# Performance work log

Hardware: AMD Instinct MI355X
Metric: run time of the kernel (lower is better)

Reference implementation:

```python
import jax, jax.numpy as jnp
import numpy as np

BS, T, NOBJ = 16, 32, 100
GLOVE, GEMB, ADIM, GCN_DIM, H, ASPACE, RES = 300, 64, 10, 512, 512, 6, 512


def setup_inputs() -> dict:
    key = jax.random.key(0)
    ks = jax.random.split(key, 34)
    rn = lambda k, shp, s=0.02: (jax.random.normal(k, shp, jnp.float32) * s)
    inp = {}
    inp["target"] = jax.random.normal(ks[0], (BS, T, GLOVE), jnp.float32)
    inp["input_"] = jax.random.normal(ks[1], (BS, T, RES, 1, 1), jnp.float32)
    inp["action_probs"] = jax.random.uniform(ks[2], (BS, T, ASPACE), jnp.float32)
    # symmetric normalized adjacency (D^-1/2 A D^-1/2), as normalize_adj produces
    A_raw = (jax.random.uniform(ks[3], (NOBJ, NOBJ)) < 0.1).astype(jnp.float32)
    A_raw = ((A_raw + A_raw.T + jnp.eye(NOBJ)) > 0).astype(jnp.float32)
    dinv = 1.0 / jnp.sqrt(jnp.sum(A_raw, axis=1))
    inp["A"] = A_raw * dinv[:, None] * dinv[None, :]
    inp["all_glove"] = jax.random.normal(ks[4], (NOBJ, GLOVE), jnp.float32)
    inp["Wword"] = rn(ks[5], (GEMB, GLOVE)); inp["bword"] = jnp.zeros((GEMB,))
    inp["Wg"] = rn(ks[6], (GEMB, GLOVE)); inp["bg"] = jnp.zeros((GEMB,))
    inp["Wa"] = rn(ks[7], (ADIM, ASPACE)); inp["ba"] = jnp.zeros((ADIM,))
    inp["W0"] = rn(ks[8], (256, RES + GEMB))
    inp["W1"] = rn(ks[9], (256, 256))
    inp["W2"] = rn(ks[10], (1, 256))
    inp["Wfm"] = rn(ks[11], (GCN_DIM, NOBJ)); inp["bfm"] = jnp.zeros((GCN_DIM,))
    fused_in = RES + GEMB + ADIM + GCN_DIM
    inp["Wf"] = rn(ks[12], (H, fused_in)); inp["bf"] = jnp.zeros((H,))
    inp["Wih"] = rn(ks[13], (4 * H, H)); inp["Whh"] = rn(ks[14], (4 * H, H))
    inp["bih"] = jnp.zeros((4 * H,)); inp["bhh"] = jnp.zeros((4 * H,))
    inp["Wa1"] = rn(ks[15], (128, H)); inp["ba1"] = jnp.zeros((128,))
    inp["Wa2"] = rn(ks[16], (ASPACE, 128)); inp["ba2"] = jnp.zeros((ASPACE,))
    inp["Wc1"] = rn(ks[17], (128, H)); inp["bc1"] = jnp.zeros((128,))
    inp["Wc2"] = rn(ks[18], (1, 128)); inp["bc2"] = jnp.zeros((1,))
    return inp


def _forward(target, input_, action_probs, A, all_glove, Wword, bword, Wg, bg,
             Wa, ba, W0, W1, W2, Wfm, bfm, Wf, bf, Wih, Whh, bih, bhh,
             Wa1, ba1, Wa2, ba2, Wc1, bc1, Wc2, bc2):
    bs, t = target.shape[0], target.shape[1]
    B = bs * t
    feats = input_.reshape(B, RES)                      # [B,512] (squeeze 1x1)
    glove_e = jax.nn.relu(target.reshape(B, GLOVE) @ Wg.T + bg)
    act_e = jax.nn.relu(action_probs.reshape(B, ASPACE) @ Wa.T + ba)
    # GCN branch (all_glove is detached in the original)
    word = jax.lax.stop_gradient(all_glove) @ Wword.T + bword   # [N,GEMB]
    N = A.shape[0]
    class_e = jnp.broadcast_to(feats[:, None, :], (B, N, RES))
    x = jnp.concatenate([class_e, jnp.broadcast_to(word[None], (B, N, GEMB))], -1)
    x = jax.nn.relu(jnp.einsum('nm,bmd->bnd', A, x) @ W0.T)     # [B,N,256]
    x = jax.nn.relu(jnp.einsum('nm,bmd->bnd', A, x) @ W1.T)     # [B,N,256]
    x = jax.nn.relu(jnp.einsum('nm,bmd->bnd', A, x) @ W2.T)     # [B,N,1]
    gcn_e = x[..., 0] @ Wfm.T + bfm                             # [B,GCN_DIM]
    fused = jnp.concatenate([feats, glove_e, act_e, gcn_e], -1)
    out = jax.nn.relu(fused @ Wf.T + bf).reshape(bs, t, H)
    # LSTM (torch gate order i,f,g,o), batch_first, zero init state
    h0 = jnp.zeros((bs, H), out.dtype)
    c0 = jnp.zeros((bs, H), out.dtype)
    def step(carry, xt):
        h, c = carry
        g = xt @ Wih.T + h @ Whh.T + bih + bhh
        i, f, gg, o = jnp.split(g, 4, axis=-1)
        c = jax.nn.sigmoid(f) * c + jax.nn.sigmoid(i) * jnp.tanh(gg)
        h = jax.nn.sigmoid(o) * jnp.tanh(c)
        return (h, c), h
    (hT, cT), hs = jax.lax.scan(step, (h0, c0), out.transpose(1, 0, 2))
    sf = hs.transpose(1, 0, 2).reshape(B, H)
    actor = jax.nn.relu(jax.nn.relu(sf @ Wa1.T + ba1) @ Wa2.T + ba2).reshape(bs, t, ASPACE)
    critic = jax.nn.relu(jax.nn.relu(sf @ Wc1.T + bc1) @ Wc2.T + bc2).reshape(bs, t, 1)
    return actor, critic, hT[None], cT[None]


def reference(target, input_, action_probs, A, all_glove, Wword, bword, Wg, bg,
              Wa, ba, W0, W1, W2, Wfm, bfm, Wf, bf, Wih, Whh, bih, bhh,
              Wa1, ba1, Wa2, ba2, Wc1, bc1, Wc2, bc2):
    return _forward(target, input_, action_probs, A, all_glove, Wword, bword,
                    Wg, bg, Wa, ba, W0, W1, W2, Wfm, bfm, Wf, bf, Wih, Whh,
                    bih, bhh, Wa1, ba1, Wa2, ba2, Wc1, bc1, Wc2, bc2)
```

## Files before the change

kernel.cpp:

```cpp
#include <hip/hip_runtime.h>
#include <cmath>

constexpr int BSZ = 16, T = 32, NOBJ = 100;
constexpr int GLOVE = 300, GEMB = 64, ADIM = 10, GCN_DIM = 512, Hh = 512, ASPACE = 6, RES = 512;
constexpr int Bt = BSZ * T;
constexpr int FUSED_IN = RES + GEMB + ADIM + GCN_DIM;
constexpr int FP = 1120;

typedef __attribute__((ext_vector_type(8))) short bf16x8;
typedef __attribute__((ext_vector_type(4))) float f32x4;

__device__ __forceinline__ unsigned short f2bf(float f) {
    unsigned u = __float_as_uint(f);
    return (unsigned short)((u + 0x7FFFu + ((u >> 16) & 1u)) >> 16);
}
__device__ __forceinline__ unsigned pk2(float a, float b) {
    return (unsigned)f2bf(a) | ((unsigned)f2bf(b) << 16);
}
__device__ __forceinline__ float sigf(float x) { return 1.f / (1.f + __expf(-x)); }

template<bool RELU, int OMODE>
__global__ __launch_bounds__(256)
void mgemm(const unsigned short* __restrict__ A, int lda,
           const unsigned short* __restrict__ B, int ldb,
           float* __restrict__ Cf, unsigned short* __restrict__ Cb, int ldc,
           const float* __restrict__ bias, int K)
{
    const int tid = threadIdx.x;
    const int l = tid & 63, wv = tid >> 6;
    const int m0 = blockIdx.y * 64 + wv * 16;
    const int n0 = blockIdx.x * 64;
    const int lr = l & 15, kg = l >> 4;
    const unsigned short* ap = A + (long)(m0 + lr) * lda + kg * 8;
    const unsigned short* bp = B + (long)(n0 + lr) * ldb + kg * 8;
    f32x4 acc0 = (f32x4){0.f, 0.f, 0.f, 0.f};
    f32x4 acc1 = acc0, acc2 = acc0, acc3 = acc0;
    for (int k0 = 0; k0 < K; k0 += 32) {
        bf16x8 a  = *(const bf16x8*)(ap + k0);
        bf16x8 b0 = *(const bf16x8*)(bp + k0);
        bf16x8 b1 = *(const bf16x8*)(bp + 16 * ldb + k0);
        bf16x8 b2 = *(const bf16x8*)(bp + 32 * ldb + k0);
        bf16x8 b3 = *(const bf16x8*)(bp + 48 * ldb + k0);
        acc0 = __builtin_amdgcn_mfma_f32_16x16x32_bf16(a, b0, acc0, 0, 0, 0);
        acc1 = __builtin_amdgcn_mfma_f32_16x16x32_bf16(a, b1, acc1, 0, 0, 0);
        acc2 = __builtin_amdgcn_mfma_f32_16x16x32_bf16(a, b2, acc2, 0, 0, 0);
        acc3 = __builtin_amdgcn_mfma_f32_16x16x32_bf16(a, b3, acc3, 0, 0, 0);
    }
    f32x4 av[4] = {acc0, acc1, acc2, acc3};
#pragma unroll
    for (int nf = 0; nf < 4; ++nf) {
        int n = n0 + nf * 16 + lr;
        float bs = bias ? bias[n] : 0.f;
#pragma unroll
        for (int r = 0; r < 4; ++r) {
            float val = av[nf][r] + bs;
            if (RELU) val = fmaxf(val, 0.f);
            long idx = (long)(m0 + kg * 4 + r) * ldc + n;
            if (OMODE == 0) Cf[idx] = val;
            else            Cb[idx] = f2bf(val);
        }
    }
}

template<bool RELU>
__global__ __launch_bounds__(128)
void gemm32(const float* __restrict__ A, int lda,
            const float* __restrict__ B, int ldb,
            float* __restrict__ C, int ldc,
            const float* __restrict__ bias, int M, int N, int K)
{
    __shared__ float As[32][36];
    __shared__ float Bs[32][68];
    const int tid = threadIdx.x;
    const int m0 = blockIdx.y * 32, n0 = blockIdx.x * 64;
    const int mi = tid >> 4, ni = tid & 15;
    float acc[4][4] = {};
    for (int k0 = 0; k0 < K; k0 += 32) {
        __syncthreads();
#pragma unroll
        for (int l = 0; l < 2; ++l) {
            int e = tid + l * 128;
            int row = e >> 3, kq = (e & 7) << 2;
            float4 va = make_float4(0.f, 0.f, 0.f, 0.f);
            if (m0 + row < M && k0 + kq < K)
                va = *(const float4*)&A[(long)(m0 + row) * lda + k0 + kq];
            As[kq + 0][row] = va.x; As[kq + 1][row] = va.y;
            As[kq + 2][row] = va.z; As[kq + 3][row] = va.w;
        }
#pragma unroll
        for (int l = 0; l < 4; ++l) {
            int e = tid + l * 128;
            int row = e >> 3, kq = (e & 7) << 2;
            float4 vb = make_float4(0.f, 0.f, 0.f, 0.f);
            if (n0 + row < N && k0 + kq < K)
                vb = *(const float4*)&B[(long)(n0 + row) * ldb + k0 + kq];
            Bs[kq + 0][row] = vb.x; Bs[kq + 1][row] = vb.y;
            Bs[kq + 2][row] = vb.z; Bs[kq + 3][row] = vb.w;
        }
        __syncthreads();
#pragma unroll
        for (int k = 0; k < 32; ++k) {
            float4 a4 = *(const float4*)&As[k][4 * mi];
            float4 b4 = *(const float4*)&Bs[k][4 * ni];
            acc[0][0] = fmaf(a4.x, b4.x, acc[0][0]); acc[0][1] = fmaf(a4.x, b4.y, acc[0][1]);
            acc[0][2] = fmaf(a4.x, b4.z, acc[0][2]); acc[0][3] = fmaf(a4.x, b4.w, acc[0][3]);
            acc[1][0] = fmaf(a4.y, b4.x, acc[1][0]); acc[1][1] = fmaf(a4.y, b4.y, acc[1][1]);
            acc[1][2] = fmaf(a4.y, b4.z, acc[1][2]); acc[1][3] = fmaf(a4.y, b4.w, acc[1][3]);
            acc[2][0] = fmaf(a4.z, b4.x, acc[2][0]); acc[2][1] = fmaf(a4.z, b4.y, acc[2][1]);
            acc[2][2] = fmaf(a4.z, b4.z, acc[2][2]); acc[2][3] = fmaf(a4.z, b4.w, acc[2][3]);
            acc[3][0] = fmaf(a4.w, b4.x, acc[3][0]); acc[3][1] = fmaf(a4.w, b4.y, acc[3][1]);
            acc[3][2] = fmaf(a4.w, b4.z, acc[3][2]); acc[3][3] = fmaf(a4.w, b4.w, acc[3][3]);
        }
    }
    const int n = n0 + 4 * ni;
    if (n >= N) return;
    float4 bv = make_float4(0.f, 0.f, 0.f, 0.f);
    if (bias) bv = *(const float4*)&bias[n];
#pragma unroll
    for (int r = 0; r < 4; ++r) {
        int m = m0 + 4 * mi + r;
        if (m >= M) continue;
        float4 v;
        v.x = acc[r][0] + bv.x; v.y = acc[r][1] + bv.y;
        v.z = acc[r][2] + bv.z; v.w = acc[r][3] + bv.w;
        if (RELU) {
            v.x = fmaxf(v.x, 0.f); v.y = fmaxf(v.y, 0.f);
            v.z = fmaxf(v.z, 0.f); v.w = fmaxf(v.w, 0.f);
        }
        *(float4*)&C[(long)m * ldc + n] = v;
    }
}

constexpr int ZLD = 152;

__global__ __launch_bounds__(256, 2)
void gcn_fused(const float* __restrict__ u,
               const float* __restrict__ v,
               const float* __restrict__ rowsum,
               const float* __restrict__ Aglob,
               const bf16x8* __restrict__ W1f,
               const bf16x8* __restrict__ Af,
               const float* __restrict__ w2,
               unsigned short* __restrict__ x3b)
{
    __shared__ unsigned short X1s[2][112 * 40];
    __shared__ unsigned short Z1Ts[128 * ZLD];
    __shared__ float u_lds[256];
    __shared__ float rs_lds[112];
    __shared__ float w2l[256];
    __shared__ float spart[4][112];
    __shared__ float sl[112];

    const int b = blockIdx.x, tid = threadIdx.x;
    const int l = tid & 63, wv = tid >> 6;
    const int lrow = l & 15, kg = l >> 4;

    u_lds[tid] = u[(long)b * 256 + tid];
    w2l[tid] = w2[tid];
    if (tid < 112) rs_lds[tid] = (tid < 100) ? rowsum[tid] : 0.f;
    if (tid < 128) {
        uint4 z = make_uint4(0, 0, 0, 0);
        *(uint4*)&Z1Ts[tid * ZLD + 112] = z;
        *(uint4*)&Z1Ts[tid * ZLD + 120] = z;
    }
    if (tid < 28) x3b[(long)b * 128 + 100 + tid] = 0;
    __syncthreads();

    const int sn = tid >> 1;
    const int kh = (tid & 1) << 4;
    const int kq = kh >> 2;
    const bool gen = (tid < 224) && (sn < 100);
    const float4* vrow = gen ? ((const float4*)v + sn * 64) : nullptr;
    const float rsn = (tid < 224) ? rs_lds[sn] : 0.f;

    float sacc[7][4];
#pragma unroll
    for (int mt = 0; mt < 7; ++mt)
#pragma unroll
        for (int r = 0; r < 4; ++r) sacc[mt][r] = 0.f;

    for (int half = 0; half < 2; ++half) {
        f32x4 acc1[7][2];
#pragma unroll
        for (int mt = 0; mt < 7; ++mt)
#pragma unroll
            for (int jtl = 0; jtl < 2; ++jtl) acc1[mt][jtl] = (f32x4){0.f, 0.f, 0.f, 0.f};

        float4 q0, q1, q2, q3;
        if (gen) { q0 = vrow[kq]; q1 = vrow[kq + 1]; q2 = vrow[kq + 2]; q3 = vrow[kq + 3]; }

        int buf = 0;
        for (int kt = 0; kt < 8; ++kt) {
            if (tid < 224) {
                int kb = kt * 32 + kh;
                uint4 p0 = make_uint4(0, 0, 0, 0), p1 = make_uint4(0, 0, 0, 0);
                if (gen) {
                    float4 u0 = *(const float4*)&u_lds[kb];
                    float4 u1 = *(const float4*)&u_lds[kb + 4];
                    float4 u2 = *(const float4*)&u_lds[kb + 8];
                    float4 u3 = *(const float4*)&u_lds[kb + 12];
                    float x0 = fmaxf(fmaf(rsn, u0.x, q0.x), 0.f), x1 = fmaxf(fmaf(rsn, u0.y, q0.y), 0.f);
                    float x2 = fmaxf(fmaf(rsn, u0.z, q0.z), 0.f), x3v = fmaxf(fmaf(rsn, u0.w, q0.w), 0.f);
                    float x4 = fmaxf(fmaf(rsn, u1.x, q1.x), 0.f), x5 = fmaxf(fmaf(rsn, u1.y, q1.y), 0.f);
                    float x6 = fmaxf(fmaf(rsn, u1.z, q1.z), 0.f), x7 = fmaxf(fmaf(rsn, u1.w, q1.w), 0.f);
                    float x8 = fmaxf(fmaf(rsn, u2.x, q2.x), 0.f), x9 = fmaxf(fmaf(rsn, u2.y, q2.y), 0.f);
                    float xa = fmaxf(fmaf(rsn, u2.z, q2.z), 0.f), xb = fmaxf(fmaf(rsn, u2.w, q2.w), 0.f);
                    float xc = fmaxf(fmaf(rsn, u3.x, q3.x), 0.f), xd = fmaxf(fmaf(rsn, u3.y, q3.y), 0.f);
                    float xe = fmaxf(fmaf(rsn, u3.z, q3.z), 0.f), xf = fmaxf(fmaf(rsn, u3.w, q3.w), 0.f);
                    p0 = make_uint4(pk2(x0, x1), pk2(x2, x3v), pk2(x4, x5), pk2(x6, x7));
                    p1 = make_uint4(pk2(x8, x9), pk2(xa, xb), pk2(xc, xd), pk2(xe, xf));
                }
                *(uint4*)&X1s[buf][sn * 40 + kh] = p0;
                *(uint4*)&X1s[buf][sn * 40 + kh + 8] = p1;
            }
            float4 n0q, n1q, n2q, n3q;
            if (kt < 7 && gen) {
                int base = (kt + 1) * 8 + kq;
                n0q = vrow[base]; n1q = vrow[base + 1]; n2q = vrow[base + 2]; n3q = vrow[base + 3];
            }
            __syncthreads();
            bf16x8 af[7];
#pragma unroll
            for (int mt = 0; mt < 7; ++mt)
                af[mt] = *(const bf16x8*)&X1s[buf][(mt * 16 + lrow) * 40 + kg * 8];
#pragma unroll
            for (int jtl = 0; jtl < 2; ++jtl) {
                int jt = half * 8 + wv * 2 + jtl;
                bf16x8 bfr = W1f[(jt * 8 + kt) * 64 + l];
#pragma unroll
                for (int mt = 0; mt < 7; ++mt)
                    acc1[mt][jtl] = __builtin_amdgcn_mfma_f32_16x16x32_bf16(af[mt], bfr, acc1[mt][jtl], 0, 0, 0);
            }
            q0 = n0q; q1 = n1q; q2 = n2q; q3 = n3q;
            buf ^= 1;
        }

#pragma unroll
        for (int mt = 0; mt < 7; ++mt)
#pragma unroll
            for (int jtl = 0; jtl < 2; ++jtl) {
                int jloc = (wv * 2 + jtl) * 16 + lrow;
                f32x4 a = acc1[mt][jtl];
                uint2 zz;
                zz.x = pk2(a[0], a[1]);
                zz.y = pk2(a[2], a[3]);
                *(uint2*)&Z1Ts[jloc * ZLD + mt * 16 + kg * 4] = zz;
            }

        bf16x8 bz[2][4];
#pragma unroll
        for (int jtl = 0; jtl < 2; ++jtl)
#pragma unroll
            for (int k2 = 0; k2 < 4; ++k2)
                bz[jtl][k2] = *(const bf16x8*)&Z1Ts[((wv * 2 + jtl) * 16 + lrow) * ZLD + k2 * 32 + kg * 8];
#pragma unroll
        for (int mt = 0; mt < 7; ++mt) {
            bf16x8 aA[4];
#pragma unroll
            for (int k2 = 0; k2 < 4; ++k2) aA[k2] = Af[(mt * 4 + k2) * 64 + l];
#pragma unroll
            for (int jtl = 0; jtl < 2; ++jtl) {
                f32x4 p = (f32x4){0.f, 0.f, 0.f, 0.f};
#pragma unroll
                for (int k2 = 0; k2 < 4; ++k2)
                    p = __builtin_amdgcn_mfma_f32_16x16x32_bf16(aA[k2], bz[jtl][k2], p, 0, 0, 0);
                float w2j = w2l[half * 128 + (wv * 2 + jtl) * 16 + lrow];
#pragma unroll
                for (int r = 0; r < 4; ++r)
                    sacc[mt][r] = fmaf(fmaxf(p[r], 0.f), w2j, sacc[mt][r]);
            }
        }
    }

#pragma unroll
    for (int mt = 0; mt < 7; ++mt) {
        float s0 = sacc[mt][0], s1 = sacc[mt][1], s2 = sacc[mt][2], s3 = sacc[mt][3];
#pragma unroll
        for (int off = 1; off < 16; off <<= 1) {
            s0 += __shfl_xor(s0, off);
            s1 += __shfl_xor(s1, off);
            s2 += __shfl_xor(s2, off);
            s3 += __shfl_xor(s3, off);
        }
        if (lrow == 0) {
            int m = mt * 16 + kg * 4;
            spart[wv][m + 0] = s0; spart[wv][m + 1] = s1;
            spart[wv][m + 2] = s2; spart[wv][m + 3] = s3;
        }
    }
    __syncthreads();
    if (tid < 112)
        sl[tid] = spart[0][tid] + spart[1][tid] + spart[2][tid] + spart[3][tid];
    __syncthreads();

    float sv0 = (l < 100) ? sl[l] : 0.f;
    float sv1 = (l + 64 < 100) ? sl[l + 64] : 0.f;
#pragma unroll 5
    for (int i = 0; i < 25; ++i) {
        int n = i * 4 + wv;
        float a0 = (l < 100) ? Aglob[n * 100 + l] : 0.f;
        float a1 = (l + 64 < 100) ? Aglob[n * 100 + l + 64] : 0.f;
        float p = a0 * sv0 + a1 * sv1;
#pragma unroll
        for (int off = 32; off; off >>= 1) p += __shfl_xor(p, off);
        if (l == 0) x3b[(long)b * 128 + n] = f2bf(fmaxf(p, 0.f));
    }
}

__global__ __launch_bounds__(256)
void lstm_mf(const float* __restrict__ xWih,
             const bf16x8* __restrict__ Whhf,
             const unsigned short* __restrict__ hPrev,
             unsigned short* __restrict__ hNext,
             float* __restrict__ cBuf,
             float* __restrict__ hFin,
             unsigned short* __restrict__ sfb, int t)
{
    __shared__ float gl[4][16][17];
    const int tid = threadIdx.x;
    const int l = tid & 63, g = tid >> 6;
    const int bid = blockIdx.x;
    const int jt = g * 32 + bid;
    const int lr = l & 15, kg = l >> 4;
    const unsigned short* hp = hPrev + lr * 512 + kg * 8;
    const bf16x8* wp = Whhf + (size_t)jt * 16 * 64 + l;
    f32x4 acc = (f32x4){0.f, 0.f, 0.f, 0.f};
#pragma unroll
    for (int kt = 0; kt < 16; ++kt) {
        bf16x8 a = *(const bf16x8*)(hp + kt * 32);
        acc = __builtin_amdgcn_mfma_f32_16x16x32_bf16(a, wp[kt * 64], acc, 0, 0, 0);
    }
#pragma unroll
    for (int r = 0; r < 4; ++r) gl[g][kg * 4 + r][lr] = acc[r];
    __syncthreads();
    const int b = tid >> 4, jl = tid & 15;
    const int jh = bid * 16 + jl;
    const float* xw = xWih + (size_t)(b * T + t) * 2048;
    float gi = gl[0][b][jl] + xw[jh];
    float gf = gl[1][b][jl] + xw[512 + jh];
    float gg = gl[2][b][jl] + xw[1024 + jh];
    float go = gl[3][b][jl] + xw[1536 + jh];
    float cp = cBuf[b * 512 + jh];
    float cn = sigf(gf) * cp + sigf(gi) * tanhf(gg);
    float hn = sigf(go) * tanhf(cn);
    cBuf[b * 512 + jh] = cn;
    hNext[b * 512 + jh] = f2bf(hn);
    hFin[b * 512 + jh] = hn;
    sfb[(size_t)(b * T + t) * 512 + jh] = f2bf(hn);
}

__global__ void k_aw_rowsum(const float* __restrict__ A, const float* __restrict__ word,
                            float* __restrict__ Aw, float* __restrict__ rowsum)
{
    int i = blockIdx.x * 256 + threadIdx.x;
    if (i < 6400) {
        int n = i / 64, k = i % 64;
        float s = 0.f;
        for (int m = 0; m < 100; ++m) s += A[n * 100 + m] * word[m * 64 + k];
        Aw[i] = s;
    } else if (i < 6500) {
        int n = i - 6400;
        float s = 0.f;
        for (int m = 0; m < 100; ++m) s += A[n * 100 + m];
        rowsum[n] = s;
    }
}

__global__ void k_prep(const float* __restrict__ Whh, uint4* __restrict__ Whhf,
                       const float* __restrict__ Wf, unsigned short* __restrict__ WfPb,
                       const float* __restrict__ Wih, unsigned short* __restrict__ Wihb,
                       const float* __restrict__ Wa1, const float* __restrict__ Wc1,
                       unsigned short* __restrict__ Whdb,
                       const float* __restrict__ ba1, const float* __restrict__ bc1,
                       float* __restrict__ bhd,
                       const float* __restrict__ Wg, unsigned short* __restrict__ Wgb,
                       const float* __restrict__ W0, unsigned short* __restrict__ W0ab,
                       const float* __restrict__ Wfm, unsigned short* __restrict__ Wfmb,
                       const float* __restrict__ target, unsigned short* __restrict__ tgtb,
                       const float* __restrict__ feats, unsigned short* __restrict__ featsb,
                       unsigned short* __restrict__ fusedb,
                       const float* __restrict__ aprob, const float* __restrict__ Wa,
                       const float* __restrict__ ba,
                       unsigned short* __restrict__ hbA, float* __restrict__ cBuf,
                       const float* __restrict__ bih, const float* __restrict__ bhh,
                       float* __restrict__ bsum,
                       const float* __restrict__ W1, uint4* __restrict__ W1f,
                       const float* __restrict__ A, uint4* __restrict__ Af)
{
    int bx = blockIdx.x, tid = threadIdx.x;
    if (bx < 512) {
        int job = bx * 256 + tid;
        int jtkt = job >> 6, ll = job & 63;
        int j = (jtkt >> 4) * 16 + (ll & 15);
        int k0 = (jtkt & 15) * 32 + (ll >> 4) * 8;
        const float* src = &Whh[(long)j * 512 + k0];
        uint4 p;
        p.x = pk2(src[0], src[1]); p.y = pk2(src[2], src[3]);
        p.z = pk2(src[4], src[5]); p.w = pk2(src[6], src[7]);
        Whhf[job] = p;
    } else if (bx < 2752) {
        int i = (bx - 512) * 256 + tid;
        int r = i / FP, c = i - r * FP;
        WfPb[i] = f2bf(c < FUSED_IN ? Wf[(long)r * FUSED_IN + c] : 0.f);
    } else if (bx < 6848) {
        int i = (bx - 2752) * 256 + tid;
        Wihb[i] = f2bf(Wih[i]);
    } else if (bx < 7360) {
        int i = (bx - 6848) * 256 + tid;
        int r = i >> 9, c = i & 511;
        Whdb[i] = f2bf(r < 128 ? Wa1[r * 512 + c] : Wc1[(r - 128) * 512 + c]);
    } else if (bx < 7361) {
        bhd[tid] = (tid < 128) ? ba1[tid] : bc1[tid - 128];
    } else if (bx < 7441) {
        int i = (bx - 7361) * 256 + tid;
        int r = i / 320, c = i - r * 320;
        Wgb[i] = f2bf(c < GLOVE ? Wg[r * GLOVE + c] : 0.f);
    } else if (bx < 7953) {
        int i = (bx - 7441) * 256 + tid;
        int r = i >> 9, c = i & 511;
        W0ab[i] = f2bf(W0[(long)r * 576 + c]);
    } else if (bx < 8209) {
        int i = (bx - 7953) * 256 + tid;
        int r = i >> 7, c = i & 127;
        Wfmb[i] = f2bf(c < 100 ? Wfm[r * 100 + c] : 0.f);
    } else if (bx < 8849) {
        int i = (bx - 8209) * 256 + tid;
        int r = i / 320, c = i - r * 320;
        tgtb[i] = f2bf(c < GLOVE ? target[(long)r * GLOVE + c] : 0.f);
    } else if (bx < 9873) {
        int i = (bx - 8849) * 256 + tid;
        featsb[i] = f2bf(feats[i]);
    } else if (bx < 10897) {
        int i = (bx - 9873) * 256 + tid;
        int r = i >> 9, c = i & 511;
        fusedb[(long)r * FP + c] = f2bf(feats[i]);
    } else if (bx < 10917) {
        int i = (bx - 10897) * 256 + tid;
        int r = i / 10, c6 = i - r * 10;
        float s = ba[c6];
#pragma unroll
        for (int k = 0; k < 6; ++k) s += aprob[r * 6 + k] * Wa[c6 * 6 + k];
        fusedb[(long)r * FP + 576 + c6] = f2bf(fmaxf(s, 0.f));
    } else if (bx < 10961) {
        int i = (bx - 10917) * 256 + tid;
        int r = i / 22, c = 1098 + (i - r * 22);
        fusedb[(long)r * FP + c] = 0;
    } else if (bx < 11009) {
        int sub = bx - 10961;
        if (sub < 16) { int i = sub * 256 + tid; hbA[i] = 0; }
        else          { int i = (sub - 16) * 256 + tid; cBuf[i] = 0.f; }
    } else if (bx < 11017) {
        int i = (bx - 11009) * 256 + tid;
        bsum[i] = bih[i] + bhh[i];
    } else if (bx < 11049) {
        int job = (bx - 11017) * 256 + tid;
        int jt = job >> 9, rem = job & 511, kt = rem >> 6, lane = rem & 63;
        int j = jt * 16 + (lane & 15), k0 = kt * 32 + (lane >> 4) * 8;
        const float* src = &W1[(long)j * 256 + k0];
        uint4 p;
        p.x = pk2(src[0], src[1]); p.y = pk2(src[2], src[3]);
        p.z = pk2(src[4], src[5]); p.w = pk2(src[6], src[7]);
        W1f[job] = p;
    } else {
        int job = (bx - 11049) * 256 + tid;
        int mt = job >> 8, rem = job & 255, kt = rem >> 6, lane = rem & 63;
        int m = mt * 16 + (lane & 15), n0 = kt * 32 + (lane >> 4) * 8;
        float h[8];
#pragma unroll
        for (int e = 0; e < 8; ++e)
            h[e] = (m < 100 && n0 + e < 100) ? A[m * 100 + n0 + e] : 0.f;
        uint4 p;
        p.x = pk2(h[0], h[1]); p.y = pk2(h[2], h[3]);
        p.z = pk2(h[4], h[5]); p.w = pk2(h[6], h[7]);
        Af[job] = p;
    }
}

__global__ void k_finish(const float* __restrict__ hd,
                         const float* __restrict__ Wa2, const float* __restrict__ ba2,
                         const float* __restrict__ Wc2, const float* __restrict__ bc2,
                         const float* __restrict__ hFin, const float* __restrict__ cBuf,
                         float* __restrict__ out)
{
    if (blockIdx.x < 32) {
        int row = blockIdx.x * 16 + (threadIdx.x >> 4);
        int slot = threadIdx.x & 15;
        if (slot < 6) {
            const float4* h4 = (const float4*)(hd + (long)row * 256);
            const float4* w4 = (const float4*)(Wa2 + slot * 128);
            float s = 0.f;
#pragma unroll
            for (int k = 0; k < 32; ++k) {
                float4 h = h4[k], w = w4[k];
                s += h.x * w.x + h.y * w.y + h.z * w.z + h.w * w.w;
            }
            out[row * 6 + slot] = fmaxf(s + ba2[slot], 0.f);
        } else if (slot == 6) {
            const float4* h4 = (const float4*)(hd + (long)row * 256 + 128);
            const float4* w4 = (const float4*)(Wc2);
            float s = 0.f;
#pragma unroll
            for (int k = 0; k < 32; ++k) {
                float4 h = h4[k], w = w4[k];
                s += h.x * w.x + h.y * w.y + h.z * w.z + h.w * w.w;
            }
            out[3072 + row] = fmaxf(s + bc2[0], 0.f);
        }
    } else {
        int i = (blockIdx.x - 32) * 256 + threadIdx.x;
        out[3584 + i] = hFin[i];
        out[11776 + i] = cBuf[i];
    }
}

static inline void mg(hipStream_t st, const unsigned short* A, int lda,
                      const unsigned short* B, int ldb,
                      float* Cf, unsigned short* Cb, int ldc,
                      const float* bias, int M, int N, int K, bool relu, bool bf16out)
{
    dim3 g(N / 64, M / 64), blk(256);
    if (bf16out) {
        if (relu) hipLaunchKernelGGL((mgemm<true, 1>), g, blk, 0, st, A, lda, B, ldb, Cf, Cb, ldc, bias, K);
        else      hipLaunchKernelGGL((mgemm<false, 1>), g, blk, 0, st, A, lda, B, ldb, Cf, Cb, ldc, bias, K);
    } else {
        if (relu) hipLaunchKernelGGL((mgemm<true, 0>), g, blk, 0, st, A, lda, B, ldb, Cf, Cb, ldc, bias, K);
        else      hipLaunchKernelGGL((mgemm<false, 0>), g, blk, 0, st, A, lda, B, ldb, Cf, Cb, ldc, bias, K);
    }
}
static inline void g32(hipStream_t st, const float* A, int lda, const float* B, int ldb,
                       float* C, int ldc, const float* bias, int M, int N, int K, bool relu)
{
    dim3 g((N + 63) / 64, (M + 31) / 32), blk(128);
    if (relu) hipLaunchKernelGGL((gemm32<true>), g, blk, 0, st, A, lda, B, ldb, C, ldc, bias, M, N, K);
    else      hipLaunchKernelGGL((gemm32<false>), g, blk, 0, st, A, lda, B, ldb, C, ldc, bias, M, N, K);
}

extern "C" void kernel_launch(void* const* d_in, const int* in_sizes, int n_in,
                              void* d_out, int out_size, void* d_ws, size_t ws_size,
                              hipStream_t stream)
{
    const float* target = (const float*)d_in[0];
    const float* input_ = (const float*)d_in[1];
    const float* aprob  = (const float*)d_in[2];
    const float* Adj    = (const float*)d_in[3];
    const float* aglove = (const float*)d_in[4];
    const float* Wword  = (const float*)d_in[5];
    const float* bword  = (const float*)d_in[6];
    const float* Wg     = (const float*)d_in[7];
    const float* bg     = (const float*)d_in[8];
    const float* Wa     = (const float*)d_in[9];
    const float* ba     = (const float*)d_in[10];
    const float* W0     = (const float*)d_in[11];
    const float* W1     = (const float*)d_in[12];
    const float* W2     = (const float*)d_in[13];
    const float* Wfm    = (const float*)d_in[14];
    const float* bfm    = (const float*)d_in[15];
    const float* Wf     = (const float*)d_in[16];
    const float* bf     = (const float*)d_in[17];
    const float* Wih    = (const float*)d_in[18];
    const float* Whh    = (const float*)d_in[19];
    const float* bih    = (const float*)d_in[20];
    const float* bhh    = (const float*)d_in[21];
    const float* Wa1    = (const float*)d_in[22];
    const float* ba1    = (const float*)d_in[23];
    const float* Wa2    = (const float*)d_in[24];
    const float* ba2    = (const float*)d_in[25];
    const float* Wc1    = (const float*)d_in[26];
    const float* bc1    = (const float*)d_in[27];
    const float* Wc2    = (const float*)d_in[28];
    const float* bc2    = (const float*)d_in[29];

    float* ws = (float*)d_ws;
    float* out = (float*)d_out;

    size_t off = 0;
    auto alloc = [&](size_t n) { size_t r = off; off += (n + 255) & ~(size_t)255; return r; };
    float* u       = ws + alloc(512 * 256);
    float* word    = ws + alloc(100 * 64);
    float* Aw      = ws + alloc(100 * 64);
    float* rowsum  = ws + alloc(128);
    float* v       = ws + alloc(100 * 256);
    float* bsum    = ws + alloc(2048);
    float* bhd     = ws + alloc(256);
    float* xWih    = ws + alloc((size_t)512 * 2048);
    float* hd      = ws + alloc(512 * 256);
    float* hFin    = ws + alloc(BSZ * Hh);
    float* cBuf    = ws + alloc(BSZ * Hh);
    float* W1frag  = ws + alloc(32768);
    float* Afrag   = ws + alloc(7168);
    float* Whhf    = ws + alloc((size_t)524288);
    unsigned short* x3b     = (unsigned short*)(ws + alloc(512 * 128 / 2));
    unsigned short* fusedb  = (unsigned short*)(ws + alloc((size_t)512 * FP / 2));
    unsigned short* WfPb    = (unsigned short*)(ws + alloc((size_t)512 * FP / 2));
    unsigned short* outfb   = (unsigned short*)(ws + alloc(512 * 512 / 2));
    unsigned short* Wihb    = (unsigned short*)(ws + alloc((size_t)2048 * 512 / 2));
    unsigned short* Whdb    = (unsigned short*)(ws + alloc(256 * 512 / 2));
    unsigned short* Wgb     = (unsigned short*)(ws + alloc(64 * 320 / 2));
    unsigned short* W0ab    = (unsigned short*)(ws + alloc(256 * 512 / 2));
    unsigned short* Wfmb    = (unsigned short*)(ws + alloc(512 * 128 / 2));
    unsigned short* tgtb    = (unsigned short*)(ws + alloc(512 * 320 / 2));
    unsigned short* featsb  = (unsigned short*)(ws + alloc(512 * 512 / 2));
    unsigned short* sfb     = (unsigned short*)(ws + alloc(512 * 512 / 2));
    unsigned short* hbA     = (unsigned short*)(ws + alloc(BSZ * Hh / 2));
    unsigned short* hbB     = (unsigned short*)(ws + alloc(BSZ * Hh / 2));
    (void)ws_size; (void)in_sizes; (void)n_in; (void)out_size;

    const float* feats = input_;

    hipLaunchKernelGGL(k_prep, dim3(11056), dim3(256), 0, stream,
                       Whh, (uint4*)Whhf, Wf, WfPb, Wih, Wihb, Wa1, Wc1, Whdb, ba1, bc1, bhd,
                       Wg, Wgb, W0, W0ab, Wfm, Wfmb, target, tgtb, feats, featsb,
                       fusedb, aprob, Wa, ba, hbA, cBuf, bih, bhh, bsum,
                       W1, (uint4*)W1frag, Adj, (uint4*)Afrag);

    g32(stream, aglove, GLOVE, Wword, GLOVE, word, 64, bword, 100, 64, GLOVE, false);
    hipLaunchKernelGGL(k_aw_rowsum, dim3(26), dim3(256), 0, stream, Adj, word, Aw, rowsum);
    g32(stream, Aw, 64, W0 + 512, 576, v, 256, nullptr, 100, 256, 64, false);

    mg(stream, featsb, 512, W0ab, 512, u, nullptr, 256, nullptr, 512, 256, 512, false, false);
    mg(stream, tgtb, 320, Wgb, 320, nullptr, fusedb + 512, FP, bg, 512, 64, 320, true, true);

    hipLaunchKernelGGL(gcn_fused, dim3(Bt), dim3(256), 0, stream,
                       u, v, rowsum, Adj, (const bf16x8*)W1frag, (const bf16x8*)Afrag, W2, x3b);
    mg(stream, x3b, 128, Wfmb, 128, nullptr, fusedb + 586, FP, bfm, 512, 512, 128, false, true);

    mg(stream, fusedb, FP, WfPb, FP, nullptr, outfb, 512, bf, 512, 512, FP, true, true);
    mg(stream, outfb, 512, Wihb, 512, xWih, nullptr, 2048, bsum, 512, 2048, 512, false, false);

    for (int t = 0; t < T; ++t) {
        const unsigned short* hp = (t & 1) ? hbB : hbA;
        unsigned short* hn = (t & 1) ? hbA : hbB;
        hipLaunchKernelGGL(lstm_mf, dim3(32), dim3(256), 0, stream,
                           xWih, (const bf16x8*)Whhf, hp, hn, cBuf, hFin, sfb, t);
    }

    mg(stream, sfb, 512, Whdb, 512, hd, nullptr, 256, bhd, 512, 256, 512, true, false);
    hipLaunchKernelGGL(k_finish, dim3(64), dim3(256), 0, stream,
                       hd, Wa2, ba2, Wc2, bc2, hFin, cBuf, out);
}
```

Measured before the change: 316.9 us.

## Persist LSTM across timesteps with grid barrier, split GCN pack, prefetch GEMM loads

The 32 per-timestep LSTM launches become a single persistent kernel. It keeps the Whh fragments and the cell state in registers and synchronises the 32 blocks through an atomic-counter grid barrier, which removes per-step launch overhead and the reloading of weights. The GCN kernel is split into a separate X1 packing kernel that writes bf16 MFMA fragments to global memory, and the core kernel reads them directly with no LDS staging or intra-loop syncs. The generic MFMA GEMM gains a 4-deep register prefetch of its operands. Risks: the spin barrier relies on all 32 blocks being co-resident, and the X1 buffer adds several MB of global traffic.

```diff
diff --git a/kernel.cpp b/kernel.cpp
--- a/kernel.cpp
+++ b/kernel.cpp
@@ -33,18 +33,39 @@
     const int lr = l & 15, kg = l >> 4;
     const unsigned short* ap = A + (long)(m0 + lr) * lda + kg * 8;
     const unsigned short* bp = B + (long)(n0 + lr) * ldb + kg * 8;
+    const int nk = K >> 5;
     f32x4 acc0 = (f32x4){0.f, 0.f, 0.f, 0.f};
     f32x4 acc1 = acc0, acc2 = acc0, acc3 = acc0;
-    for (int k0 = 0; k0 < K; k0 += 32) {
-        bf16x8 a  = *(const bf16x8*)(ap + k0);
-        bf16x8 b0 = *(const bf16x8*)(bp + k0);
-        bf16x8 b1 = *(const bf16x8*)(bp + 16 * ldb + k0);
-        bf16x8 b2 = *(const bf16x8*)(bp + 32 * ldb + k0);
-        bf16x8 b3 = *(const bf16x8*)(bp + 48 * ldb + k0);
-        acc0 = __builtin_amdgcn_mfma_f32_16x16x32_bf16(a, b0, acc0, 0, 0, 0);
-        acc1 = __builtin_amdgcn_mfma_f32_16x16x32_bf16(a, b1, acc1, 0, 0, 0);
-        acc2 = __builtin_amdgcn_mfma_f32_16x16x32_bf16(a, b2, acc2, 0, 0, 0);
-        acc3 = __builtin_amdgcn_mfma_f32_16x16x32_bf16(a, b3, acc3, 0, 0, 0);
+    bf16x8 a_[4], b0_[4], b1_[4], b2_[4], b3_[4];
+#pragma unroll
+    for (int s = 0; s < 4; ++s) {
+        if (s < nk) {
+            int k = s * 32;
+            a_[s]  = *(const bf16x8*)(ap + k);
+            b0_[s] = *(const bf16x8*)(bp + k);
+            b1_[s] = *(const bf16x8*)(bp + 16 * ldb + k);
+            b2_[s] = *(const bf16x8*)(bp + 32 * ldb + k);
+            b3_[s] = *(const bf16x8*)(bp + 48 * ldb + k);
+        }
+    }
+    for (int i = 0; i < nk; i += 4) {
+#pragma unroll
+        for (int s = 0; s < 4; ++s) {
+            if (i + s < nk) {
+                acc0 = __builtin_amdgcn_mfma_f32_16x16x32_bf16(a_[s], b0_[s], acc0, 0, 0, 0);
+                acc1 = __builtin_amdgcn_mfma_f32_16x16x32_bf16(a_[s], b1_[s], acc1, 0, 0, 0);
+                acc2 = __builtin_amdgcn_mfma_f32_16x16x32_bf16(a_[s], b2_[s], acc2, 0, 0, 0);
+                acc3 = __builtin_amdgcn_mfma_f32_16x16x32_bf16(a_[s], b3_[s], acc3, 0, 0, 0);
+                if (i + s + 4 < nk) {
+                    int k = (i + s + 4) * 32;
+                    a_[s]  = *(const bf16x8*)(ap + k);
+                    b0_[s] = *(const bf16x8*)(bp + k);
+                    b1_[s] = *(const bf16x8*)(bp + 16 * ldb + k);
+                    b2_[s] = *(const bf16x8*)(bp + 32 * ldb + k);
+                    b3_[s] = *(const bf16x8*)(bp + 48 * ldb + k);
+                }
+            }
+        }
     }
     f32x4 av[4] = {acc0, acc1, acc2, acc3};
 #pragma unroll
@@ -131,22 +152,53 @@
     }
 }
 
-constexpr int ZLD = 152;
-
-__global__ __launch_bounds__(256, 2)
-void gcn_fused(const float* __restrict__ u,
-               const float* __restrict__ v,
-               const float* __restrict__ rowsum,
-               const float* __restrict__ Aglob,
-               const bf16x8* __restrict__ W1f,
-               const bf16x8* __restrict__ Af,
-               const float* __restrict__ w2,
-               unsigned short* __restrict__ x3b)
-{
-    __shared__ unsigned short X1s[2][112 * 40];
-    __shared__ unsigned short Z1Ts[128 * ZLD];
+__global__ __launch_bounds__(256)
+void x1pack(const float* __restrict__ u, const float* __restrict__ v,
+            const float* __restrict__ rowsum, uint4* __restrict__ X1g)
+{
     __shared__ float u_lds[256];
     __shared__ float rs_lds[112];
+    const int b = blockIdx.x, tid = threadIdx.x;
+    u_lds[tid] = u[(long)b * 256 + tid];
+    if (tid < 112) rs_lds[tid] = (tid < 100) ? rowsum[tid] : 0.f;
+    __syncthreads();
+    uint4* outp = X1g + (size_t)b * 3584;
+#pragma unroll
+    for (int it = 0; it < 14; ++it) {
+        int job = it * 256 + tid;
+        int l = job & 63;
+        int kt = (job >> 6) & 7;
+        int mt = job >> 9;
+        int n = mt * 16 + (l & 15);
+        int k0 = kt * 32 + ((l >> 4) << 3);
+        uint4 p = make_uint4(0, 0, 0, 0);
+        if (n < 100) {
+            float rsn = rs_lds[n];
+            float4 u0 = *(const float4*)&u_lds[k0];
+            float4 u1 = *(const float4*)&u_lds[k0 + 4];
+            const float4* vp = (const float4*)&v[n * 256 + k0];
+            float4 v0 = vp[0], v1 = vp[1];
+            float x0 = fmaxf(fmaf(rsn, u0.x, v0.x), 0.f), x1 = fmaxf(fmaf(rsn, u0.y, v0.y), 0.f);
+            float x2 = fmaxf(fmaf(rsn, u0.z, v0.z), 0.f), x3 = fmaxf(fmaf(rsn, u0.w, v0.w), 0.f);
+            float x4 = fmaxf(fmaf(rsn, u1.x, v1.x), 0.f), x5 = fmaxf(fmaf(rsn, u1.y, v1.y), 0.f);
+            float x6 = fmaxf(fmaf(rsn, u1.z, v1.z), 0.f), x7 = fmaxf(fmaf(rsn, u1.w, v1.w), 0.f);
+            p = make_uint4(pk2(x0, x1), pk2(x2, x3), pk2(x4, x5), pk2(x6, x7));
+        }
+        outp[job] = p;
+    }
+}
+
+constexpr int ZLD = 152;
+
+__global__ __launch_bounds__(256, 2)
+void gcn_core(const bf16x8* __restrict__ X1g,
+              const float* __restrict__ Aglob,
+              const bf16x8* __restrict__ W1f,
+              const bf16x8* __restrict__ Af,
+              const float* __restrict__ w2,
+              unsigned short* __restrict__ x3b)
+{
+    __shared__ unsigned short Z1Ts[128 * ZLD];
     __shared__ float w2l[256];
     __shared__ float spart[4][112];
     __shared__ float sl[112];
@@ -155,9 +207,7 @@
     const int l = tid & 63, wv = tid >> 6;
     const int lrow = l & 15, kg = l >> 4;
 
-    u_lds[tid] = u[(long)b * 256 + tid];
     w2l[tid] = w2[tid];
-    if (tid < 112) rs_lds[tid] = (tid < 100) ? rowsum[tid] : 0.f;
     if (tid < 128) {
         uint4 z = make_uint4(0, 0, 0, 0);
         *(uint4*)&Z1Ts[tid * ZLD + 112] = z;
@@ -166,12 +216,7 @@
     if (tid < 28) x3b[(long)b * 128 + 100 + tid] = 0;
     __syncthreads();
 
-    const int sn = tid >> 1;
-    const int kh = (tid & 1) << 4;
-    const int kq = kh >> 2;
-    const bool gen = (tid < 224) && (sn < 100);
-    const float4* vrow = gen ? ((const float4*)v + sn * 64) : nullptr;
-    const float rsn = (tid < 224) ? rs_lds[sn] : 0.f;
+    const bf16x8* xb = X1g + (size_t)b * 3584 + l;
 
     float sacc[7][4];
 #pragma unroll
@@ -186,43 +231,12 @@
 #pragma unroll
             for (int jtl = 0; jtl < 2; ++jtl) acc1[mt][jtl] = (f32x4){0.f, 0.f, 0.f, 0.f};
 
-        float4 q0, q1, q2, q3;
-        if (gen) { q0 = vrow[kq]; q1 = vrow[kq + 1]; q2 = vrow[kq + 2]; q3 = vrow[kq + 3]; }
-
-        int buf = 0;
+#pragma unroll
         for (int kt = 0; kt < 8; ++kt) {
-            if (tid < 224) {
-                int kb = kt * 32 + kh;
-                uint4 p0 = make_uint4(0, 0, 0, 0), p1 = make_uint4(0, 0, 0, 0);
-                if (gen) {
-                    float4 u0 = *(const float4*)&u_lds[kb];
-                    float4 u1 = *(const float4*)&u_lds[kb + 4];
-                    float4 u2 = *(const float4*)&u_lds[kb + 8];
-                    float4 u3 = *(const float4*)&u_lds[kb + 12];
-                    float x0 = fmaxf(fmaf(rsn, u0.x, q0.x), 0.f), x1 = fmaxf(fmaf(rsn, u0.y, q0.y), 0.f);
-                    float x2 = fmaxf(fmaf(rsn, u0.z, q0.z), 0.f), x3v = fmaxf(fmaf(rsn, u0.w, q0.w), 0.f);
-                    float x4 = fmaxf(fmaf(rsn, u1.x, q1.x), 0.f), x5 = fmaxf(fmaf(rsn, u1.y, q1.y), 0.f);
-                    float x6 = fmaxf(fmaf(rsn, u1.z, q1.z), 0.f), x7 = fmaxf(fmaf(rsn, u1.w, q1.w), 0.f);
-                    float x8 = fmaxf(fmaf(rsn, u2.x, q2.x), 0.f), x9 = fmaxf(fmaf(rsn, u2.y, q2.y), 0.f);
-                    float xa = fmaxf(fmaf(rsn, u2.z, q2.z), 0.f), xb = fmaxf(fmaf(rsn, u2.w, q2.w), 0.f);
-                    float xc = fmaxf(fmaf(rsn, u3.x, q3.x), 0.f), xd = fmaxf(fmaf(rsn, u3.y, q3.y), 0.f);
-                    float xe = fmaxf(fmaf(rsn, u3.z, q3.z), 0.f), xf = fmaxf(fmaf(rsn, u3.w, q3.w), 0.f);
-                    p0 = make_uint4(pk2(x0, x1), pk2(x2, x3v), pk2(x4, x5), pk2(x6, x7));
-                    p1 = make_uint4(pk2(x8, x9), pk2(xa, xb), pk2(xc, xd), pk2(xe, xf));
-                }
-                *(uint4*)&X1s[buf][sn * 40 + kh] = p0;
-                *(uint4*)&X1s[buf][sn * 40 + kh + 8] = p1;
-            }
-            float4 n0q, n1q, n2q, n3q;
-            if (kt < 7 && gen) {
-                int base = (kt + 1) * 8 + kq;
-                n0q = vrow[base]; n1q = vrow[base + 1]; n2q = vrow[base + 2]; n3q = vrow[base + 3];
-            }
-            __syncthreads();
             bf16x8 af[7];
 #pragma unroll
             for (int mt = 0; mt < 7; ++mt)
-                af[mt] = *(const bf16x8*)&X1s[buf][(mt * 16 + lrow) * 40 + kg * 8];
+                af[mt] = xb[mt * 512 + kt * 64];
 #pragma unroll
             for (int jtl = 0; jtl < 2; ++jtl) {
                 int jt = half * 8 + wv * 2 + jtl;
@@ -231,8 +245,6 @@
                 for (int mt = 0; mt < 7; ++mt)
                     acc1[mt][jtl] = __builtin_amdgcn_mfma_f32_16x16x32_bf16(af[mt], bfr, acc1[mt][jtl], 0, 0, 0);
             }
-            q0 = n0q; q1 = n1q; q2 = n2q; q3 = n3q;
-            buf ^= 1;
         }
 
 #pragma unroll
@@ -308,13 +320,14 @@
 }
 
 __global__ __launch_bounds__(256)
-void lstm_mf(const float* __restrict__ xWih,
-             const bf16x8* __restrict__ Whhf,
-             const unsigned short* __restrict__ hPrev,
-             unsigned short* __restrict__ hNext,
-             float* __restrict__ cBuf,
-             float* __restrict__ hFin,
-             unsigned short* __restrict__ sfb, int t)
+void lstm_persist(const float* __restrict__ xWih,
+                  const bf16x8* __restrict__ Whhf,
+                  unsigned short* __restrict__ hbA,
+                  unsigned short* __restrict__ hbB,
+                  float* __restrict__ cBuf,
+                  float* __restrict__ hFin,
+                  unsigned short* __restrict__ sfb,
+                  unsigned* __restrict__ bar)
 {
     __shared__ float gl[4][16][17];
     const int tid = threadIdx.x;
@@ -322,31 +335,48 @@
     const int bid = blockIdx.x;
     const int jt = g * 32 + bid;
     const int lr = l & 15, kg = l >> 4;
-    const unsigned short* hp = hPrev + lr * 512 + kg * 8;
     const bf16x8* wp = Whhf + (size_t)jt * 16 * 64 + l;
-    f32x4 acc = (f32x4){0.f, 0.f, 0.f, 0.f};
-#pragma unroll
-    for (int kt = 0; kt < 16; ++kt) {
-        bf16x8 a = *(const bf16x8*)(hp + kt * 32);
-        acc = __builtin_amdgcn_mfma_f32_16x16x32_bf16(a, wp[kt * 64], acc, 0, 0, 0);
-    }
-#pragma unroll
-    for (int r = 0; r < 4; ++r) gl[g][kg * 4 + r][lr] = acc[r];
-    __syncthreads();
-    const int b = tid >> 4, jl = tid & 15;
+    bf16x8 w[16];
+#pragma unroll
+    for (int kt = 0; kt < 16; ++kt) w[kt] = wp[kt * 64];
+    const int fb = tid >> 4, jl = tid & 15;
     const int jh = bid * 16 + jl;
-    const float* xw = xWih + (size_t)(b * T + t) * 2048;
-    float gi = gl[0][b][jl] + xw[jh];
-    float gf = gl[1][b][jl] + xw[512 + jh];
-    float gg = gl[2][b][jl] + xw[1024 + jh];
-    float go = gl[3][b][jl] + xw[1536 + jh];
-    float cp = cBuf[b * 512 + jh];
-    float cn = sigf(gf) * cp + sigf(gi) * tanhf(gg);
-    float hn = sigf(go) * tanhf(cn);
-    cBuf[b * 512 + jh] = cn;
-    hNext[b * 512 + jh] = f2bf(hn);
-    hFin[b * 512 + jh] = hn;
-    sfb[(size_t)(b * T + t) * 512 + jh] = f2bf(hn);
+    float c_reg = 0.f;
+    const unsigned short* hprev = hbA;
+    unsigned short* hnext = hbB;
+    for (int t = 0; t < T; ++t) {
+        const unsigned short* hp = hprev + lr * 512 + kg * 8;
+        f32x4 acc = (f32x4){0.f, 0.f, 0.f, 0.f};
+#pragma unroll
+        for (int kt = 0; kt < 16; ++kt) {
+            bf16x8 a = *(const bf16x8*)(hp + kt * 32);
+            acc = __builtin_amdgcn_mfma_f32_16x16x32_bf16(a, w[kt], acc, 0, 0, 0);
+        }
+#pragma unroll
+        for (int r = 0; r < 4; ++r) gl[g][kg * 4 + r][lr] = acc[r];
+        __syncthreads();
+        const float* xw = xWih + (size_t)(fb * T + t) * 2048;
+        float gi = gl[0][fb][jl] + xw[jh];
+        float gf = gl[1][fb][jl] + xw[512 + jh];
+        float gg = gl[2][fb][jl] + xw[1024 + jh];
+        float go = gl[3][fb][jl] + xw[1536 + jh];
+        float cn = sigf(gf) * c_reg + sigf(gi) * tanhf(gg);
+        float hn = sigf(go) * tanhf(cn);
+        c_reg = cn;
+        hnext[fb * 512 + jh] = f2bf(hn);
+        sfb[(size_t)(fb * T + t) * 512 + jh] = f2bf(hn);
+        if (t == T - 1) { hFin[fb * 512 + jh] = hn; cBuf[fb * 512 + jh] = cn; }
+        __syncthreads();
+        if (tid == 0) {
+            __threadfence();
+            atomicAdd(bar, 1u);
+            unsigned target = 32u * (unsigned)(t + 1);
+            while (atomicAdd(bar, 0u) < target) { }
+            __threadfence();
+        }
+        __syncthreads();
+        const unsigned short* tmp = hprev; hprev = hnext; hnext = (unsigned short*)tmp;
+    }
 }
 
 __global__ void k_aw_rowsum(const float* __restrict__ A, const float* __restrict__ word,
@@ -381,7 +411,7 @@
                        unsigned short* __restrict__ fusedb,
                        const float* __restrict__ aprob, const float* __restrict__ Wa,
                        const float* __restrict__ ba,
-                       unsigned short* __restrict__ hbA, float* __restrict__ cBuf,
+                       unsigned short* __restrict__ hbA, unsigned* __restrict__ bar,
                        const float* __restrict__ bih, const float* __restrict__ bhh,
                        float* __restrict__ bsum,
                        const float* __restrict__ W1, uint4* __restrict__ W1f,
@@ -445,15 +475,16 @@
         int i = (bx - 10917) * 256 + tid;
         int r = i / 22, c = 1098 + (i - r * 22);
         fusedb[(long)r * FP + c] = 0;
-    } else if (bx < 11009) {
-        int sub = bx - 10961;
-        if (sub < 16) { int i = sub * 256 + tid; hbA[i] = 0; }
-        else          { int i = (sub - 16) * 256 + tid; cBuf[i] = 0.f; }
-    } else if (bx < 11017) {
-        int i = (bx - 11009) * 256 + tid;
+    } else if (bx < 10993) {
+        int i = (bx - 10961) * 256 + tid;
+        hbA[i] = 0;
+    } else if (bx < 10994) {
+        if (tid == 0) bar[0] = 0u;
+    } else if (bx < 11002) {
+        int i = (bx - 10994) * 256 + tid;
         bsum[i] = bih[i] + bhh[i];
-    } else if (bx < 11049) {
-        int job = (bx - 11017) * 256 + tid;
+    } else if (bx < 11034) {
+        int job = (bx - 11002) * 256 + tid;
         int jt = job >> 9, rem = job & 511, kt = rem >> 6, lane = rem & 63;
         int j = jt * 16 + (lane & 15), k0 = kt * 32 + (lane >> 4) * 8;
         const float* src = &W1[(long)j * 256 + k0];
@@ -462,7 +493,7 @@
         p.z = pk2(src[4], src[5]); p.w = pk2(src[6], src[7]);
         W1f[job] = p;
     } else {
-        int job = (bx - 11049) * 256 + tid;
+        int job = (bx - 11034) * 256 + tid;
         int mt = job >> 8, rem = job & 255, kt = rem >> 6, lane = rem & 63;
         int m = mt * 16 + (lane & 15), n0 = kt * 32 + (lane >> 4) * 8;
         float h[8];
@@ -589,6 +620,8 @@
     float* W1frag  = ws + alloc(32768);
     float* Afrag   = ws + alloc(7168);
     float* Whhf    = ws + alloc((size_t)524288);
+    float* X1gf    = ws + alloc((size_t)512 * 3584 * 4);
+    unsigned* bar  = (unsigned*)(ws + alloc(256));
     unsigned short* x3b     = (unsigned short*)(ws + alloc(512 * 128 / 2));
     unsigned short* fusedb  = (unsigned short*)(ws + alloc((size_t)512 * FP / 2));
     unsigned short* WfPb    = (unsigned short*)(ws + alloc((size_t)512 * FP / 2));
@@ -607,10 +640,10 @@
 
     const float* feats = input_;
 
-    hipLaunchKernelGGL(k_prep, dim3(11056), dim3(256), 0, stream,
+    hipLaunchKernelGGL(k_prep, dim3(11041), dim3(256), 0, stream,
                        Whh, (uint4*)Whhf, Wf, WfPb, Wih, Wihb, Wa1, Wc1, Whdb, ba1, bc1, bhd,
                        Wg, Wgb, W0, W0ab, Wfm, Wfmb, target, tgtb, feats, featsb,
-                       fusedb, aprob, Wa, ba, hbA, cBuf, bih, bhh, bsum,
+                       fusedb, aprob, Wa, ba, hbA, bar, bih, bhh, bsum,
                        W1, (uint4*)W1frag, Adj, (uint4*)Afrag);
 
     g32(stream, aglove, GLOVE, Wword, GLOVE, word, 64, bword, 100, 64, GLOVE, false);
@@ -620,19 +653,16 @@
     mg(stream, featsb, 512, W0ab, 512, u, nullptr, 256, nullptr, 512, 256, 512, false, false);
     mg(stream, tgtb, 320, Wgb, 320, nullptr, fusedb + 512, FP, bg, 512, 64, 320, true, true);
 
-    hipLaunchKernelGGL(gcn_fused, dim3(Bt), dim3(256), 0, stream,
-                       u, v, rowsum, Adj, (const bf16x8*)W1frag, (const bf16x8*)Afrag, W2, x3b);
+    hipLaunchKernelGGL(x1pack, dim3(Bt), dim3(256), 0, stream, u, v, rowsum, (uint4*)X1gf);
+    hipLaunchKernelGGL(gcn_core, dim3(Bt), dim3(256), 0, stream,
+                       (const bf16x8*)X1gf, Adj, (const bf16x8*)W1frag, (const bf16x8*)Afrag, W2, x3b);
     mg(stream, x3b, 128, Wfmb, 128, nullptr, fusedb + 586, FP, bfm, 512, 512, 128, false, true);
 
     mg(stream, fusedb, FP, WfPb, FP, nullptr, outfb, 512, bf, 512, 512, FP, true, true);
     mg(stream, outfb, 512, Wihb, 512, xWih, nullptr, 2048, bsum, 512, 2048, 512, false, false);
 
-    for (int t = 0; t < T; ++t) {
-        const unsigned short* hp = (t & 1) ? hbB : hbA;
-        unsigned short* hn = (t & 1) ? hbA : hbB;
-        hipLaunchKernelGGL(lstm_mf, dim3(32), dim3(256), 0, stream,
-                           xWih, (const bf16x8*)Whhf, hp, hn, cBuf, hFin, sfb, t);
-    }
+    hipLaunchKernelGGL(lstm_persist, dim3(32), dim3(256), 0, stream,
+                       xWih, (const bf16x8*)Whhf, hbA, hbB, cBuf, hFin, sfb, bar);
 
     mg(stream, sfb, 512, Whdb, 512, hd, nullptr, 256, bhd, 512, 256, 512, true, false);
     hipLaunchKernelGGL(k_finish, dim3(64), dim3(256), 0, stream,
```

After: 380.5 us, median of 4. 20.0% more time.
